# Kernel optimization log

Measured on AMD Instinct MI355X. Metric: run time of the kernel, lower is better.

## Reference

```python
import jax, jax.numpy as jnp
import numpy as np

N, E, C0, H, NC = 50000, 800000, 64, 64, 2500
NUM_LAYERS = 3


def setup_inputs() -> dict:
    key = jax.random.key(0)
    ks = jax.random.split(key, 16)
    inp = {}
    inp["x"] = jax.random.normal(ks[0], (N, C0), dtype=jnp.float32)
    inp["edge_index"] = jax.random.randint(ks[1], (2, E), 0, N, dtype=jnp.int64)
    inp["cluster"] = jax.random.randint(ks[2], (N,), 0, NC, dtype=jnp.int64)
    c = C0
    for i in range(NUM_LAYERS):
        inp[f"w1_{i}"] = jax.random.normal(ks[3 + 4 * i], (c, H), jnp.float32) / np.sqrt(c).astype(np.float32)
        inp[f"b1_{i}"] = jnp.zeros((H,), jnp.float32)
        inp[f"w2_{i}"] = jax.random.normal(ks[4 + 4 * i], (H, c), jnp.float32) / np.sqrt(H).astype(np.float32)
        inp[f"b2_{i}"] = jnp.zeros((c,), jnp.float32)
        c *= 2
    inp["n_clusters"] = NC
    return inp


def _glp(x, src, dst, w1, b1, w2, b2, num_nodes):
    # node encoder MLP: Linear -> ReLU -> Linear
    h = jnp.maximum(x @ w1 + b1, 0.0) @ w2 + b2  # [N, c]
    # message passing: gather at source, scatter-max at destination
    msg = h[src]  # [E, c]
    aggr = jax.ops.segment_max(msg, dst, num_segments=num_nodes)  # [N, c]
    # nodes with no incoming edges -> 0 (PyG fill for max aggregation)
    aggr = jnp.where(jnp.isfinite(aggr), aggr, 0.0)
    # update: concat(encoder_out, aggregated) -> channels double
    return jnp.concatenate([h, aggr], axis=1)


def reference(x, edge_index, cluster,
              w1_0, b1_0, w2_0, b2_0,
              w1_1, b1_1, w2_1, b2_1,
              w1_2, b1_2, w2_2, b2_2,
              n_clusters):
    num_nodes = x.shape[0]
    src, dst = edge_index[0], edge_index[1]
    params = [(w1_0, b1_0, w2_0, b2_0), (w1_1, b1_1, w2_1, b2_1), (w1_2, b1_2, w2_2, b2_2)]
    for (w1, b1, w2, b2) in params:
        x = _glp(x, src, dst, w1, b1, w2, b2, num_nodes)
    # cluster-wise max pool over polylines
    pooled = jax.ops.segment_max(x, cluster, num_segments=n_clusters)  # [NC, 512]
    pooled = jnp.where(jnp.isfinite(pooled), pooled, 0.0)
    # column-wise (dim=0) normalization as in the source
    out = pooled / (jnp.linalg.norm(pooled, axis=0) + 1e-6)
    return out
```

## Files before the change

### kernel.cpp

```cpp
#include <hip/hip_runtime.h>
#include <math.h>

typedef unsigned short bfu;
typedef __attribute__((ext_vector_type(8))) short bf16x8;
typedef __attribute__((ext_vector_type(16))) float f32x16;

__device__ __forceinline__ float b2f(bfu u) {
    unsigned int x = ((unsigned int)u) << 16;
    return __uint_as_float(x);
}
__device__ __forceinline__ bfu f2bf(float f) {
    unsigned int u = __float_as_uint(f);
    unsigned int r = (u + 0x7FFFu + ((u >> 16) & 1u)) >> 16;
    return (bfu)r;
}

struct InitArgs {
    int* deg; int N; int* cdeg; int NC; float* sumsq;
    const float* w[6]; bfu* whi[6]; bfu* wlo[6]; int K[6]; int Nw[6];
    const float* x0; bfu* xhi; bfu* xlo; int xtotal;
};

__global__ __launch_bounds__(256) void k_init(InitArgs a) {
    const int j = blockIdx.y;
    const int g0 = blockIdx.x * 256 + threadIdx.x;
    const int gs = gridDim.x * 256;
    if (j == 0) {
        for (int i = g0; i < a.N; i += gs) a.deg[i] = 0;
        for (int i = g0; i < a.NC; i += gs) a.cdeg[i] = 0;
        for (int i = g0; i < 512; i += gs) a.sumsq[i] = 0.f;
    } else if (j <= 6) {
        const int jj = j - 1;
        const int K = a.K[jj], Nw = a.Nw[jj];
        const int total = K * Nw;
        const float* w = a.w[jj];
        bfu* dhi = a.whi[jj];
        bfu* dlo = a.wlo[jj];
        for (int idx = g0; idx < total; idx += gs) {
            int k = idx / Nw, n = idx % Nw;
            float v = w[idx];
            bfu hi = f2bf(v);
            bfu lo = f2bf(v - b2f(hi));
            dhi[n * K + k] = hi;
            dlo[n * K + k] = lo;
        }
    } else {
        for (int i = g0; i * 4 < a.xtotal; i += gs) {
            int base = i * 4;
            float4 v = *(const float4*)&a.x0[base];
            ushort4 h, l;
            h.x = f2bf(v.x); l.x = f2bf(v.x - b2f(h.x));
            h.y = f2bf(v.y); l.y = f2bf(v.y - b2f(h.y));
            h.z = f2bf(v.z); l.z = f2bf(v.z - b2f(h.z));
            h.w = f2bf(v.w); l.w = f2bf(v.w - b2f(h.w));
            *(ushort4*)&a.xhi[base] = h;
            *(ushort4*)&a.xlo[base] = l;
        }
    }
}

__global__ void k_hist2(const int* __restrict__ dst, int E, int* __restrict__ deg,
                        const int* __restrict__ cluster, int N, int* __restrict__ cdeg) {
    int i = blockIdx.x * blockDim.x + threadIdx.x;
    if (i < E) atomicAdd(&deg[dst[i]], 1);
    if (i < N) atomicAdd(&cdeg[cluster[i]], 1);
}

__global__ __launch_bounds__(256) void k_scanA(const int* __restrict__ deg, int N,
                                               const int* __restrict__ cdeg, int NC,
                                               int* __restrict__ scn0, int* __restrict__ scn1,
                                               int* __restrict__ bsum0, int* __restrict__ bsum1) {
    __shared__ int part[256];
    const int seg = blockIdx.y;
    const int n = seg ? NC : N;
    const int* d = seg ? cdeg : deg;
    int* scn = seg ? scn1 : scn0;
    int* bs  = seg ? bsum1 : bsum0;
    const int b = blockIdx.x;
    if (b * 256 >= n) return;
    const int t = threadIdx.x;
    const int i = b * 256 + t;
    int v = (i < n) ? d[i] : 0;
    part[t] = v;
    __syncthreads();
#pragma unroll
    for (int off = 1; off < 256; off <<= 1) {
        int cv = part[t];
        int u = (t >= off) ? part[t - off] : 0;
        __syncthreads();
        part[t] = cv + u;
        __syncthreads();
    }
    if (i < n) scn[i] = part[t];
    if (t == 255) bs[b] = part[255];
}

__global__ __launch_bounds__(256) void k_scanC(const int* __restrict__ deg, int N,
                                               const int* __restrict__ cdeg, int NC,
                                               const int* __restrict__ scn0, const int* __restrict__ scn1,
                                               const int* __restrict__ bsum0, int nb0,
                                               const int* __restrict__ bsum1, int nb1,
                                               int* __restrict__ ptr0, int* __restrict__ cur0,
                                               int* __restrict__ ptr1, int* __restrict__ cur1) {
    __shared__ int part[256];
    const int seg = blockIdx.y;
    const int n = seg ? NC : N;
    const int nb = seg ? nb1 : nb0;
    const int* d = seg ? cdeg : deg;
    const int* scn = seg ? scn1 : scn0;
    const int* bsum = seg ? bsum1 : bsum0;
    int* ptr = seg ? ptr1 : ptr0;
    int* cur = seg ? cur1 : cur0;
    const int b = blockIdx.x;
    if (b * 256 >= n) return;
    const int t = threadIdx.x;
    int v = (t < nb) ? bsum[t] : 0;
    part[t] = v;
    __syncthreads();
#pragma unroll
    for (int off = 1; off < 256; off <<= 1) {
        int cv = part[t];
        int u = (t >= off) ? part[t - off] : 0;
        __syncthreads();
        part[t] = cv + u;
        __syncthreads();
    }
    const int boff = (b == 0) ? 0 : part[b - 1];
    const int i = b * 256 + t;
    if (i < n) {
        int e = boff + scn[i] - d[i];
        ptr[i] = e;
        cur[i] = e;
    }
    if (b == 0 && t == 0) ptr[n] = part[nb - 1];
}

__global__ void k_scatter2(const int* __restrict__ dst, const int* __restrict__ src, int E,
                           int* __restrict__ cur, int* __restrict__ colidx,
                           const int* __restrict__ cluster, int N,
                           int* __restrict__ ccur, int* __restrict__ cidx) {
    int i = blockIdx.x * blockDim.x + threadIdx.x;
    if (i < E) {
        int d = dst[i];
        int pos = atomicAdd(&cur[d], 1);
        colidx[pos] = src[i];
    }
    if (i < N) {
        int c = cluster[i];
        int pos = atomicAdd(&ccur[c], 1);
        cidx[pos] = i;
    }
}

__device__ __forceinline__ int swz(int row, int kb) {
    return (row * 128 + (kb ^ ((row & 7) << 4))) >> 1;
}

template <bool WLO>
__global__ __launch_bounds__(256) void k_layer(const bfu* __restrict__ Ahi, const bfu* __restrict__ Alo,
                                               const bfu* __restrict__ W1hi, const bfu* __restrict__ W1lo,
                                               const float* __restrict__ b1,
                                               const bfu* __restrict__ W2hi, const bfu* __restrict__ W2lo,
                                               const float* __restrict__ b2,
                                               bfu* __restrict__ Ohi, bfu* __restrict__ Olo,
                                               int M, int K, int Kzero, int Nw2, int OS) {
    __shared__ __align__(16) bfu As[2][64 * 64];
    __shared__ __align__(16) bfu Bs[2][64 * 64];
    const int tid = threadIdx.x;
    const int wave = tid >> 6, lane = tid & 63;
    const int m0 = blockIdx.x * 64;
    const int l31 = lane & 31;
    const int khalfb = (lane >> 5) * 16;
    const int arow = (wave & 1) * 32 + l31;
    const int cbase = (wave >> 1) * 32;

    f32x16 acc;
#pragma unroll
    for (int i = 0; i < 16; i++) acc[i] = 0.f;

    for (int k0 = 0; k0 < K; k0 += 64) {
        const bool full3 = (k0 < Kzero);
#pragma unroll
        for (int i = 0; i < 2; i++) {
            int idx = i * 2048 + tid * 8;
            int row = idx >> 6;
            int ke = idx & 63;
            int gm = m0 + row; if (gm >= M) gm = M - 1;
            uint4 v = *(const uint4*)&Ahi[(size_t)gm * K + k0 + ke];
            *(uint4*)&As[0][swz(row, ke * 2)] = v;
        }
        if (full3) {
#pragma unroll
            for (int i = 0; i < 2; i++) {
                int idx = i * 2048 + tid * 8;
                int row = idx >> 6;
                int ke = idx & 63;
                int gm = m0 + row; if (gm >= M) gm = M - 1;
                uint4 v = *(const uint4*)&Alo[(size_t)gm * K + k0 + ke];
                *(uint4*)&As[1][swz(row, ke * 2)] = v;
            }
        }
#pragma unroll
        for (int p = 0; p < 2; p++) {
            const bfu* src = p ? W1lo : W1hi;
#pragma unroll
            for (int i = 0; i < 2; i++) {
                int idx = i * 2048 + tid * 8;
                int row = idx >> 6;
                int ke = idx & 63;
                uint4 v = *(const uint4*)&src[(size_t)row * K + k0 + ke];
                *(uint4*)&Bs[p][swz(row, ke * 2)] = v;
            }
        }
        __syncthreads();
#pragma unroll
        for (int s = 0; s < 4; s++) {
            int kb = s * 32 + khalfb;
            bf16x8 ah = *(const bf16x8*)&As[0][swz(arow, kb)];
            bf16x8 bh = *(const bf16x8*)&Bs[0][swz(cbase + l31, kb)];
            bf16x8 bl = *(const bf16x8*)&Bs[1][swz(cbase + l31, kb)];
            acc = __builtin_amdgcn_mfma_f32_32x32x16_bf16(ah, bh, acc, 0, 0, 0);
            acc = __builtin_amdgcn_mfma_f32_32x32x16_bf16(ah, bl, acc, 0, 0, 0);
            if (full3) {
                bf16x8 al = *(const bf16x8*)&As[1][swz(arow, kb)];
                acc = __builtin_amdgcn_mfma_f32_32x32x16_bf16(al, bh, acc, 0, 0, 0);
            }
        }
        __syncthreads();
    }

    {
        float bc = b1[cbase + l31];
        const int rbase = (wave & 1) * 32 + 4 * (lane >> 5);
#pragma unroll
        for (int r = 0; r < 16; r++) {
            int row = rbase + (r & 3) + 8 * (r >> 2);
            float t0 = fmaxf(acc[r] + bc, 0.f);
            bfu h0 = f2bf(t0);
            bfu l0 = f2bf(t0 - b2f(h0));
            As[0][swz(row, (cbase + l31) * 2)] = h0;
            As[1][swz(row, (cbase + l31) * 2)] = l0;
        }
    }

    for (int n0 = 0; n0 < Nw2; n0 += 64) {
        __syncthreads();
#pragma unroll
        for (int p = 0; p < 2; p++) {
            const bfu* src = p ? W2lo : W2hi;
#pragma unroll
            for (int i = 0; i < 2; i++) {
                int idx = i * 2048 + tid * 8;
                int row = idx >> 6;
                int ke = idx & 63;
                uint4 v = *(const uint4*)&src[(size_t)(n0 + row) * 64 + ke];
                *(uint4*)&Bs[p][swz(row, ke * 2)] = v;
            }
        }
        __syncthreads();
#pragma unroll
        for (int i = 0; i < 16; i++) acc[i] = 0.f;
#pragma unroll
        for (int s = 0; s < 4; s++) {
            int kb = s * 32 + khalfb;
            bf16x8 th = *(const bf16x8*)&As[0][swz(arow, kb)];
            bf16x8 tl = *(const bf16x8*)&As[1][swz(arow, kb)];
            bf16x8 wh = *(const bf16x8*)&Bs[0][swz(cbase + l31, kb)];
            bf16x8 wl = *(const bf16x8*)&Bs[1][swz(cbase + l31, kb)];
            acc = __builtin_amdgcn_mfma_f32_32x32x16_bf16(th, wh, acc, 0, 0, 0);
            acc = __builtin_amdgcn_mfma_f32_32x32x16_bf16(th, wl, acc, 0, 0, 0);
            acc = __builtin_amdgcn_mfma_f32_32x32x16_bf16(tl, wh, acc, 0, 0, 0);
        }
        float bc = b2[n0 + cbase + l31];
        const int rbase = m0 + (wave & 1) * 32 + 4 * (lane >> 5);
#pragma unroll
        for (int r = 0; r < 16; r++) {
            int grow = rbase + (r & 3) + 8 * (r >> 2);
            if (grow < M) {
                float o0 = acc[r] + bc;
                bfu h0 = f2bf(o0);
                size_t base = (size_t)grow * OS + n0 + cbase;
                Ohi[base + l31] = h0;
                if (WLO) {
                    Olo[base + l31] = f2bf(o0 - b2f(h0));
                }
            }
        }
    }
}

template <int R>
__device__ __forceinline__ void gmax(const bfu* __restrict__ p, float* acc) {
    if (R == 4) {
        ushort4 v = *(const ushort4*)p;
        acc[0] = fmaxf(acc[0], b2f(v.x)); acc[1] = fmaxf(acc[1], b2f(v.y));
        acc[2] = fmaxf(acc[2], b2f(v.z)); acc[3] = fmaxf(acc[3], b2f(v.w));
    } else if (R == 2) {
        ushort2 v = *(const ushort2*)p;
        acc[0] = fmaxf(acc[0], b2f(v.x)); acc[1] = fmaxf(acc[1], b2f(v.y));
    } else {
        acc[0] = fmaxf(acc[0], b2f(*p));
    }
}

template <int R>
__global__ void k_agg(const bfu* __restrict__ hplane, bfu* __restrict__ whi,
                      const int* __restrict__ rowptr, const int* __restrict__ colidx,
                      int N, int stride) {
    const int wid = (blockIdx.x * blockDim.x + threadIdx.x) >> 6;
    const int lane = threadIdx.x & 63;
    if (wid >= N) return;
    const int beg = rowptr[wid], end = rowptr[wid + 1];
    const int ch = lane * R;

    float acc[R];
#pragma unroll
    for (int r = 0; r < R; r++) acc[r] = -INFINITY;

    int i = beg;
    for (; i + 8 <= end; i += 8) {
        int off[8];
#pragma unroll
        for (int u = 0; u < 8; u++) off[u] = colidx[i + u] * stride + ch;
#pragma unroll
        for (int u = 0; u < 8; u++) gmax<R>(hplane + off[u], acc);
    }
    for (; i + 2 <= end; i += 2) {
        int o0 = colidx[i] * stride + ch;
        int o1 = colidx[i + 1] * stride + ch;
        gmax<R>(hplane + o0, acc);
        gmax<R>(hplane + o1, acc);
    }
    if (i < end) gmax<R>(hplane + colidx[i] * stride + ch, acc);

    if (beg == end) {
#pragma unroll
        for (int r = 0; r < R; r++) acc[r] = 0.f;
    }
    int obase = wid * stride + 64 * R + ch;
#pragma unroll
    for (int r = 0; r < R; r++) whi[obase + r] = f2bf(acc[r]);
}

__global__ void k_pool(const bfu* __restrict__ xhi,
                       const int* __restrict__ cptr, const int* __restrict__ cidx,
                       float* __restrict__ pooled) {
    int cl = blockIdx.x;
    int tid = threadIdx.x;
    int beg = cptr[cl], end = cptr[cl + 1];
    float ax = -INFINITY, ay = -INFINITY;
    int i = beg;
    for (; i + 4 <= end; i += 4) {
        ushort2 h0 = *(const ushort2*)&xhi[cidx[i + 0] * 512 + tid * 2];
        ushort2 h1 = *(const ushort2*)&xhi[cidx[i + 1] * 512 + tid * 2];
        ushort2 h2 = *(const ushort2*)&xhi[cidx[i + 2] * 512 + tid * 2];
        ushort2 h3 = *(const ushort2*)&xhi[cidx[i + 3] * 512 + tid * 2];
        ax = fmaxf(ax, fmaxf(fmaxf(b2f(h0.x), b2f(h1.x)), fmaxf(b2f(h2.x), b2f(h3.x))));
        ay = fmaxf(ay, fmaxf(fmaxf(b2f(h0.y), b2f(h1.y)), fmaxf(b2f(h2.y), b2f(h3.y))));
    }
    for (; i < end; i++) {
        ushort2 h = *(const ushort2*)&xhi[cidx[i] * 512 + tid * 2];
        ax = fmaxf(ax, b2f(h.x)); ay = fmaxf(ay, b2f(h.y));
    }
    if (beg == end) { ax = 0.f; ay = 0.f; }
    float2 o; o.x = ax; o.y = ay;
    *(float2*)&pooled[(size_t)cl * 512 + tid * 2] = o;
}

__global__ void k_sumsq(const float* __restrict__ pooled, float* __restrict__ sumsq, int NC) {
    int tid = threadIdx.x;
    float ax = 0.f, ay = 0.f;
    for (int r = blockIdx.x; r < NC; r += gridDim.x) {
        float2 v = *(const float2*)&pooled[(size_t)r * 512 + tid * 2];
        ax += v.x * v.x; ay += v.y * v.y;
    }
    atomicAdd(&sumsq[tid * 2 + 0], ax);
    atomicAdd(&sumsq[tid * 2 + 1], ay);
}

__global__ void k_scale(const float* __restrict__ pooled, const float* __restrict__ sumsq,
                        float* __restrict__ out, int total) {
    int i = blockIdx.x * blockDim.x + threadIdx.x;
    int base = i * 4;
    if (base < total) {
        float4 v = *(const float4*)&pooled[base];
        int col = base & 511;
        v.x /= (sqrtf(sumsq[col + 0]) + 1e-6f);
        v.y /= (sqrtf(sumsq[col + 1]) + 1e-6f);
        v.z /= (sqrtf(sumsq[col + 2]) + 1e-6f);
        v.w /= (sqrtf(sumsq[col + 3]) + 1e-6f);
        *(float4*)&out[base] = v;
    }
}

extern "C" void kernel_launch(void* const* d_in, const int* in_sizes, int n_in,
                              void* d_out, int out_size, void* d_ws, size_t ws_size,
                              hipStream_t stream) {
    const float* x0      = (const float*)d_in[0];
    const int*   ei      = (const int*)d_in[1];
    const int*   cluster = (const int*)d_in[2];
    const float* w1_[3] = {(const float*)d_in[3], (const float*)d_in[7],  (const float*)d_in[11]};
    const float* b1_[3] = {(const float*)d_in[4], (const float*)d_in[8],  (const float*)d_in[12]};
    const float* w2_[3] = {(const float*)d_in[5], (const float*)d_in[9],  (const float*)d_in[13]};
    const float* b2_[3] = {(const float*)d_in[6], (const float*)d_in[10], (const float*)d_in[14]};

    const int N  = in_sizes[2];
    const int E  = in_sizes[1] / 2;
    const int NC = 2500;
    float* out = (float*)d_out;

    char* p = (char*)d_ws;
    auto alloc = [&](size_t bytes) -> char* {
        char* r = p;
        p += (bytes + 255) & ~(size_t)255;
        return r;
    };
    bfu* X0hi = (bfu*)alloc((size_t)N * 64 * 2);
    bfu* X0lo = (bfu*)alloc((size_t)N * 64 * 2);
    bfu* X1hi = (bfu*)alloc((size_t)N * 128 * 2);
    bfu* X1lo = (bfu*)alloc((size_t)N * 128 * 2);
    bfu* X2hi = (bfu*)alloc((size_t)N * 256 * 2);
    bfu* X2lo = (bfu*)alloc((size_t)N * 256 * 2);
    bfu* X3hi = (bfu*)alloc((size_t)N * 512 * 2);
    bfu* w1t_hi[3]; bfu* w1t_lo[3]; bfu* w2t_hi[3]; bfu* w2t_lo[3];
    const int Ks[3] = {64, 128, 256};
    for (int l = 0; l < 3; l++) {
        w1t_hi[l] = (bfu*)alloc((size_t)64 * Ks[l] * 2);
        w1t_lo[l] = (bfu*)alloc((size_t)64 * Ks[l] * 2);
        w2t_hi[l] = (bfu*)alloc((size_t)Ks[l] * 64 * 2);
        w2t_lo[l] = (bfu*)alloc((size_t)Ks[l] * 64 * 2);
    }
    float* pooled = (float*)alloc((size_t)NC * 512 * 4);
    float* sumsq  = (float*)alloc(512 * 4);
    int*   deg    = (int*)alloc((size_t)(N + 1) * 4);
    int*   rowptr = (int*)alloc((size_t)(N + 1) * 4);
    int*   cursor = (int*)alloc((size_t)(N + 1) * 4);
    int*   colidx = (int*)alloc((size_t)E * 4);
    int*   cdeg   = (int*)alloc((size_t)(NC + 1) * 4);
    int*   cptr   = (int*)alloc((size_t)(NC + 1) * 4);
    int*   ccur   = (int*)alloc((size_t)(NC + 1) * 4);
    int*   cidx   = (int*)alloc((size_t)N * 4);
    int*   scn0   = (int*)alloc((size_t)N * 4);
    int*   scn1   = (int*)alloc((size_t)NC * 4);
    int*   bsum0  = (int*)alloc(256 * 4);
    int*   bsum1  = (int*)alloc(256 * 4);

    const int* src = ei;
    const int* dst = ei + E;

    InitArgs ia;
    ia.deg = deg; ia.N = N; ia.cdeg = cdeg; ia.NC = NC; ia.sumsq = sumsq;
    for (int l = 0; l < 3; l++) {
        ia.w[2 * l]     = w1_[l]; ia.whi[2 * l]     = w1t_hi[l]; ia.wlo[2 * l]     = w1t_lo[l];
        ia.K[2 * l]     = Ks[l];  ia.Nw[2 * l]      = 64;
        ia.w[2 * l + 1] = w2_[l]; ia.whi[2 * l + 1] = w2t_hi[l]; ia.wlo[2 * l + 1] = w2t_lo[l];
        ia.K[2 * l + 1] = 64;     ia.Nw[2 * l + 1]  = Ks[l];
    }
    ia.x0 = x0; ia.xhi = X0hi; ia.xlo = X0lo; ia.xtotal = N * 64;
    k_init<<<dim3(128, 8), 256, 0, stream>>>(ia);

    k_hist2<<<(E + 255) / 256, 256, 0, stream>>>(dst, E, deg, cluster, N, cdeg);

    const int nb0 = (N + 255) / 256;
    const int nb1 = (NC + 255) / 256;
    k_scanA<<<dim3(nb0, 2), 256, 0, stream>>>(deg, N, cdeg, NC, scn0, scn1, bsum0, bsum1);
    k_scanC<<<dim3(nb0, 2), 256, 0, stream>>>(deg, N, cdeg, NC, scn0, scn1, bsum0, nb0, bsum1, nb1,
                                              rowptr, cursor, cptr, ccur);

    k_scatter2<<<(E + 255) / 256, 256, 0, stream>>>(dst, src, E, cursor, colidx,
                                                    cluster, N, ccur, cidx);

    const int Mt = (N + 63) / 64;
    const int aggBlocks = (N * 64 + 255) / 256;

    k_layer<true><<<Mt, 256, 0, stream>>>(X0hi, X0lo, w1t_hi[0], w1t_lo[0], b1_[0],
                                          w2t_hi[0], w2t_lo[0], b2_[0], X1hi, X1lo,
                                          N, 64, 64, 64, 128);
    k_agg<1><<<aggBlocks, 256, 0, stream>>>(X1hi, X1hi, rowptr, colidx, N, 128);

    k_layer<true><<<Mt, 256, 0, stream>>>(X1hi, X1lo, w1t_hi[1], w1t_lo[1], b1_[1],
                                          w2t_hi[1], w2t_lo[1], b2_[1], X2hi, X2lo,
                                          N, 128, 64, 128, 256);
    k_agg<2><<<aggBlocks, 256, 0, stream>>>(X2hi, X2hi, rowptr, colidx, N, 256);

    k_layer<false><<<Mt, 256, 0, stream>>>(X2hi, X2lo, w1t_hi[2], w1t_lo[2], b1_[2],
                                           w2t_hi[2], w2t_lo[2], b2_[2], X3hi, nullptr,
                                           N, 256, 128, 256, 512);
    k_agg<4><<<aggBlocks, 256, 0, stream>>>(X3hi, X3hi, rowptr, colidx, N, 512);

    k_pool<<<NC, 256, 0, stream>>>(X3hi, cptr, cidx, pooled);
    k_sumsq<<<64, 256, 0, stream>>>(pooled, sumsq, NC);
    k_scale<<<(out_size / 4 + 255) / 256, 256, 0, stream>>>(pooled, sumsq, out, out_size);
}
```

Baseline: 307.1 us.

## Fuse CSR scatter into layer-0 MLP kernel and coarsen histogram threads

Adds a combined kernel whose first Mt blocks run the layer-0 MLP (a specialization of k_layer with fixed sizes) and whose extra blocks perform the edge and cluster CSR scatter. The two independent jobs overlap and one launch is removed. The histogram kernel now handles four elements per thread, cutting the block count. Shared memory is declared for the scatter blocks too, which may limit occupancy, and the MLP copy duplicates code.

```diff
diff --git a/kernel.cpp b/kernel.cpp
--- a/kernel.cpp
+++ b/kernel.cpp
@@ -61,9 +61,17 @@
 
 __global__ void k_hist2(const int* __restrict__ dst, int E, int* __restrict__ deg,
                         const int* __restrict__ cluster, int N, int* __restrict__ cdeg) {
-    int i = blockIdx.x * blockDim.x + threadIdx.x;
-    if (i < E) atomicAdd(&deg[dst[i]], 1);
-    if (i < N) atomicAdd(&cdeg[cluster[i]], 1);
+    const int base = blockIdx.x * 1024 + threadIdx.x;
+#pragma unroll
+    for (int u = 0; u < 4; u++) {
+        int e = base + u * 256;
+        if (e < E) atomicAdd(&deg[dst[e]], 1);
+    }
+#pragma unroll
+    for (int u = 0; u < 4; u++) {
+        int i = base + u * 256;
+        if (i < N) atomicAdd(&cdeg[cluster[i]], 1);
+    }
 }
 
 __global__ __launch_bounds__(256) void k_scanA(const int* __restrict__ deg, int N,
@@ -135,25 +143,163 @@
     if (b == 0 && t == 0) ptr[n] = part[nb - 1];
 }
 
-__global__ void k_scatter2(const int* __restrict__ dst, const int* __restrict__ src, int E,
-                           int* __restrict__ cur, int* __restrict__ colidx,
-                           const int* __restrict__ cluster, int N,
-                           int* __restrict__ ccur, int* __restrict__ cidx) {
-    int i = blockIdx.x * blockDim.x + threadIdx.x;
-    if (i < E) {
-        int d = dst[i];
-        int pos = atomicAdd(&cur[d], 1);
-        colidx[pos] = src[i];
-    }
-    if (i < N) {
-        int c = cluster[i];
-        int pos = atomicAdd(&ccur[c], 1);
-        cidx[pos] = i;
-    }
-}
-
 __device__ __forceinline__ int swz(int row, int kb) {
     return (row * 128 + (kb ^ ((row & 7) << 4))) >> 1;
+}
+
+__global__ __launch_bounds__(256) void k_l0scat(const bfu* __restrict__ Ahi, const bfu* __restrict__ Alo,
+                                                const bfu* __restrict__ W1hi, const bfu* __restrict__ W1lo,
+                                                const float* __restrict__ b1,
+                                                const bfu* __restrict__ W2hi, const bfu* __restrict__ W2lo,
+                                                const float* __restrict__ b2,
+                                                bfu* __restrict__ Ohi, bfu* __restrict__ Olo,
+                                                int M, int Mt,
+                                                const int* __restrict__ dst, const int* __restrict__ src, int E,
+                                                int* __restrict__ cur, int* __restrict__ colidx,
+                                                const int* __restrict__ cluster,
+                                                int* __restrict__ ccur, int* __restrict__ cidx) {
+    __shared__ __align__(16) bfu As[2][64 * 64];
+    __shared__ __align__(16) bfu Bs[2][64 * 64];
+    const int tid = threadIdx.x;
+
+    if (blockIdx.x >= Mt) {
+        const int base = (blockIdx.x - Mt) * 1024 + tid;
+#pragma unroll
+        for (int u = 0; u < 4; u++) {
+            int e = base + u * 256;
+            if (e < E) {
+                int d = dst[e];
+                int pos = atomicAdd(&cur[d], 1);
+                colidx[pos] = src[e];
+            }
+        }
+#pragma unroll
+        for (int u = 0; u < 4; u++) {
+            int i = base + u * 256;
+            if (i < M) {
+                int c = cluster[i];
+                int pos = atomicAdd(&ccur[c], 1);
+                cidx[pos] = i;
+            }
+        }
+        return;
+    }
+
+    const int K = 64, Nw2 = 64, OS = 128;
+    const int wave = tid >> 6, lane = tid & 63;
+    const int m0 = blockIdx.x * 64;
+    const int l31 = lane & 31;
+    const int khalfb = (lane >> 5) * 16;
+    const int arow = (wave & 1) * 32 + l31;
+    const int cbase = (wave >> 1) * 32;
+
+    f32x16 acc;
+#pragma unroll
+    for (int i = 0; i < 16; i++) acc[i] = 0.f;
+
+    {
+        const int k0 = 0;
+#pragma unroll
+        for (int i = 0; i < 2; i++) {
+            int idx = i * 2048 + tid * 8;
+            int row = idx >> 6;
+            int ke = idx & 63;
+            int gm = m0 + row; if (gm >= M) gm = M - 1;
+            uint4 v = *(const uint4*)&Ahi[(size_t)gm * K + k0 + ke];
+            *(uint4*)&As[0][swz(row, ke * 2)] = v;
+        }
+#pragma unroll
+        for (int i = 0; i < 2; i++) {
+            int idx = i * 2048 + tid * 8;
+            int row = idx >> 6;
+            int ke = idx & 63;
+            int gm = m0 + row; if (gm >= M) gm = M - 1;
+            uint4 v = *(const uint4*)&Alo[(size_t)gm * K + k0 + ke];
+            *(uint4*)&As[1][swz(row, ke * 2)] = v;
+        }
+#pragma unroll
+        for (int p = 0; p < 2; p++) {
+            const bfu* srcw = p ? W1lo : W1hi;
+#pragma unroll
+            for (int i = 0; i < 2; i++) {
+                int idx = i * 2048 + tid * 8;
+                int row = idx >> 6;
+                int ke = idx & 63;
+                uint4 v = *(const uint4*)&srcw[(size_t)row * K + k0 + ke];
+                *(uint4*)&Bs[p][swz(row, ke * 2)] = v;
+            }
+        }
+        __syncthreads();
+#pragma unroll
+        for (int s = 0; s < 4; s++) {
+            int kb = s * 32 + khalfb;
+            bf16x8 ah = *(const bf16x8*)&As[0][swz(arow, kb)];
+            bf16x8 bh = *(const bf16x8*)&Bs[0][swz(cbase + l31, kb)];
+            bf16x8 bl = *(const bf16x8*)&Bs[1][swz(cbase + l31, kb)];
+            bf16x8 al = *(const bf16x8*)&As[1][swz(arow, kb)];
+            acc = __builtin_amdgcn_mfma_f32_32x32x16_bf16(ah, bh, acc, 0, 0, 0);
+            acc = __builtin_amdgcn_mfma_f32_32x32x16_bf16(ah, bl, acc, 0, 0, 0);
+            acc = __builtin_amdgcn_mfma_f32_32x32x16_bf16(al, bh, acc, 0, 0, 0);
+        }
+        __syncthreads();
+    }
+
+    {
+        float bc = b1[cbase + l31];
+        const int rbase = (wave & 1) * 32 + 4 * (lane >> 5);
+#pragma unroll
+        for (int r = 0; r < 16; r++) {
+            int row = rbase + (r & 3) + 8 * (r >> 2);
+            float t0 = fmaxf(acc[r] + bc, 0.f);
+            bfu h0 = f2bf(t0);
+            bfu l0 = f2bf(t0 - b2f(h0));
+            As[0][swz(row, (cbase + l31) * 2)] = h0;
+            As[1][swz(row, (cbase + l31) * 2)] = l0;
+        }
+    }
+
+    for (int n0 = 0; n0 < Nw2; n0 += 64) {
+        __syncthreads();
+#pragma unroll
+        for (int p = 0; p < 2; p++) {
+            const bfu* srcw = p ? W2lo : W2hi;
+#pragma unroll
+            for (int i = 0; i < 2; i++) {
+                int idx = i * 2048 + tid * 8;
+                int row = idx >> 6;
+                int ke = idx & 63;
+                uint4 v = *(const uint4*)&srcw[(size_t)(n0 + row) * 64 + ke];
+                *(uint4*)&Bs[p][swz(row, ke * 2)] = v;
+            }
+        }
+        __syncthreads();
+#pragma unroll
+        for (int i = 0; i < 16; i++) acc[i] = 0.f;
+#pragma unroll
+        for (int s = 0; s < 4; s++) {
+            int kb = s * 32 + khalfb;
+            bf16x8 th = *(const bf16x8*)&As[0][swz(arow, kb)];
+            bf16x8 tl = *(const bf16x8*)&As[1][swz(arow, kb)];
+            bf16x8 wh = *(const bf16x8*)&Bs[0][swz(cbase + l31, kb)];
+            bf16x8 wl = *(const bf16x8*)&Bs[1][swz(cbase + l31, kb)];
+            acc = __builtin_amdgcn_mfma_f32_32x32x16_bf16(th, wh, acc, 0, 0, 0);
+            acc = __builtin_amdgcn_mfma_f32_32x32x16_bf16(th, wl, acc, 0, 0, 0);
+            acc = __builtin_amdgcn_mfma_f32_32x32x16_bf16(tl, wh, acc, 0, 0, 0);
+        }
+        float bc = b2[n0 + cbase + l31];
+        const int rbase = m0 + (wave & 1) * 32 + 4 * (lane >> 5);
+#pragma unroll
+        for (int r = 0; r < 16; r++) {
+            int grow = rbase + (r & 3) + 8 * (r >> 2);
+            if (grow < M) {
+                float o0 = acc[r] + bc;
+                bfu h0 = f2bf(o0);
+                size_t base = (size_t)grow * OS + n0 + cbase;
+                Ohi[base + l31] = h0;
+                Olo[base + l31] = f2bf(o0 - b2f(h0));
+            }
+        }
+    }
 }
 
 template <bool WLO>
@@ -459,7 +605,7 @@
     ia.x0 = x0; ia.xhi = X0hi; ia.xlo = X0lo; ia.xtotal = N * 64;
     k_init<<<dim3(128, 8), 256, 0, stream>>>(ia);
 
-    k_hist2<<<(E + 255) / 256, 256, 0, stream>>>(dst, E, deg, cluster, N, cdeg);
+    k_hist2<<<(E + 1023) / 1024, 256, 0, stream>>>(dst, E, deg, cluster, N, cdeg);
 
     const int nb0 = (N + 255) / 256;
     const int nb1 = (NC + 255) / 256;
@@ -467,15 +613,15 @@
     k_scanC<<<dim3(nb0, 2), 256, 0, stream>>>(deg, N, cdeg, NC, scn0, scn1, bsum0, nb0, bsum1, nb1,
                                               rowptr, cursor, cptr, ccur);
 
-    k_scatter2<<<(E + 255) / 256, 256, 0, stream>>>(dst, src, E, cursor, colidx,
-                                                    cluster, N, ccur, cidx);
-
     const int Mt = (N + 63) / 64;
+    const int Sc = (E + 1023) / 1024;
     const int aggBlocks = (N * 64 + 255) / 256;
 
-    k_layer<true><<<Mt, 256, 0, stream>>>(X0hi, X0lo, w1t_hi[0], w1t_lo[0], b1_[0],
+    k_l0scat<<<Mt + Sc, 256, 0, stream>>>(X0hi, X0lo, w1t_hi[0], w1t_lo[0], b1_[0],
                                           w2t_hi[0], w2t_lo[0], b2_[0], X1hi, X1lo,
-                                          N, 64, 64, 64, 128);
+                                          N, Mt,
+                                          dst, src, E, cursor, colidx,
+                                          cluster, ccur, cidx);
     k_agg<1><<<aggBlocks, 256, 0, stream>>>(X1hi, X1hi, rowptr, colidx, N, 128);
 
     k_layer<true><<<Mt, 256, 0, stream>>>(X1hi, X1lo, w1t_hi[1], w1t_lo[1], b1_[1],
```

After: 312.1 us. Within noise of the previous version (+1.6%).
